# Kernel tuning notes

Hardware: AMD Instinct MI355X
Metric: run time of the kernel (lower is better)

The kernel has to match this reference:

```python
import jax, jax.numpy as jnp
import numpy as np

B, S, IN, H = 32, 512, 512, 1024

def setup_inputs() -> dict:
    key = jax.random.key(0)
    ks = jax.random.split(key, 13)
    sx = 1.0 / np.sqrt(IN)
    sh = 1.0 / np.sqrt(H)
    inp = {"x": jax.random.normal(ks[0], (B, S, IN), dtype=jnp.float32)}
    names_x = ["wxf", "wxi", "wxo", "wxc"]
    names_h = ["whf", "whi", "who", "whc"]
    names_b = ["bhf", "bhi", "bho", "bhc"]
    for j in range(4):
        inp[names_x[j]] = jax.random.uniform(ks[1 + j], (IN, H), dtype=jnp.float32, minval=-sx, maxval=sx)
        inp[names_h[j]] = jax.random.uniform(ks[5 + j], (H, H), dtype=jnp.float32, minval=-sh, maxval=sh)
        inp[names_b[j]] = jax.random.uniform(ks[9 + j], (H,), dtype=jnp.float32, minval=-sh, maxval=sh)
    return inp

def reference(x, wxf, whf, bhf, wxi, whi, bhi, wxo, who, bho, wxc, whc, bhc):
    b = x.shape[0]
    h = whf.shape[0]
    # Precompute all input projections (no bias on w_x_*): [S, B, 4H]
    wx = jnp.concatenate([wxf, wxi, wxo, wxc], axis=1)          # [IN, 4H]
    gx = jnp.einsum("bsi,ig->sbg", x, wx)                        # [S, B, 4H]
    wh = jnp.concatenate([whf, whi, who, whc], axis=1)           # [H, 4H]
    bh = jnp.concatenate([bhf, bhi, bho, bhc], axis=0)           # [4H]

    h0 = jnp.zeros((b, h), dtype=x.dtype)
    c0 = jnp.zeros((b, h), dtype=x.dtype)

    def step(carry, gxt):
        ht, ct = carry
        gates = gxt + ht @ wh + bh                               # [B, 4H]
        ft, it, ot, ch = jnp.split(jax.nn.sigmoid(gates), 4, axis=-1)
        # NOTE: original uses sigmoid (not tanh) for the candidate cell ct_hat
        ct_new = ft * ct + it * ch
        ht_new = ot * jnp.tanh(ct_new)
        # NOTE: original appends the output gate ot (not ht) to the sequence
        return (ht_new, ct_new), ot

    (ht, ct), outs = jax.lax.scan(step, (h0, c0), gx)
    return jnp.transpose(outs, (1, 0, 2)), (ht, ct)
```

## Files before the change

### kernel.cpp

```cpp
#include <hip/hip_runtime.h>
#include <stdint.h>


typedef short bf16x8 __attribute__((ext_vector_type(8)));
typedef float f32x4  __attribute__((ext_vector_type(4)));
typedef unsigned int uint4v __attribute__((ext_vector_type(4)));

#define MFMA16(a, b, c) __builtin_amdgcn_mfma_f32_16x16x32_bf16((a), (b), (c), 0, 0, 0)

__device__ __forceinline__ unsigned short f2bf(float f) {
    unsigned int u = __builtin_bit_cast(unsigned int, f);
    u = (u + 0x7FFFu + ((u >> 16) & 1u)) >> 16;
    return (unsigned short)u;
}
__device__ __forceinline__ float bf2f(unsigned short h) {
    unsigned int u = ((unsigned int)h) << 16;
    return __builtin_bit_cast(float, u);
}
__device__ __forceinline__ float sigmoidf_(float x) { return 1.0f / (1.0f + __expf(-x)); }
__device__ __forceinline__ float tanhf_(float x)    { return 1.0f - 2.0f / (__expf(2.0f * x) + 1.0f); }

__global__ void __launch_bounds__(256) gx_gemm(
    const float* __restrict__ X,
    const float* __restrict__ Wf, const float* __restrict__ Wi,
    const float* __restrict__ Wo, const float* __restrict__ Wc,
    unsigned short* __restrict__ gxOut)
{
    __shared__ unsigned short As[128 * 40];
    __shared__ unsigned short Bs[128 * 40];

    const int tid  = threadIdx.x;
    const int lane = tid & 63;
    const int wid  = tid >> 6;
    const int lr   = lane & 15;
    const int lq   = lane >> 4;

    const int m0 = blockIdx.x * 128;
    const int n0 = blockIdx.y * 128;
    const float* Wg = (n0 < 1024) ? Wf : (n0 < 2048) ? Wi : (n0 < 3072) ? Wo : Wc;
    const int ncol0 = n0 & 1023;

    const int mw = (wid & 1) * 64;
    const int nw = (wid >> 1) * 64;

    f32x4 acc[4][4];
#pragma unroll
    for (int i = 0; i < 4; i++)
#pragma unroll
        for (int j = 0; j < 4; j++) acc[i][j] = (f32x4){0.f, 0.f, 0.f, 0.f};

    for (int k0 = 0; k0 < 512; k0 += 32) {
#pragma unroll
        for (int i = 0; i < 4; i++) {
            int s   = tid + i * 256;
            int row = s >> 3;
            int c4  = s & 7;
            float4 v = *(const float4*)(X + (size_t)(m0 + row) * 512 + k0 + c4 * 4);
            ushort4 h;
            h.x = f2bf(v.x); h.y = f2bf(v.y); h.z = f2bf(v.z); h.w = f2bf(v.w);
            *(ushort4*)(As + row * 40 + c4 * 4) = h;
        }
#pragma unroll
        for (int i = 0; i < 4; i++) {
            int s  = tid + i * 256;
            int kk = s >> 5;
            int c4 = s & 31;
            float4 v = *(const float4*)(Wg + (size_t)(k0 + kk) * 1024 + ncol0 + c4 * 4);
            Bs[(c4 * 4 + 0) * 40 + kk] = f2bf(v.x);
            Bs[(c4 * 4 + 1) * 40 + kk] = f2bf(v.y);
            Bs[(c4 * 4 + 2) * 40 + kk] = f2bf(v.z);
            Bs[(c4 * 4 + 3) * 40 + kk] = f2bf(v.w);
        }
        __syncthreads();

        bf16x8 af[4], bfr[4];
#pragma unroll
        for (int tm = 0; tm < 4; tm++)
            af[tm] = *(const bf16x8*)(As + (mw + tm * 16 + lr) * 40 + lq * 8);
#pragma unroll
        for (int tn = 0; tn < 4; tn++)
            bfr[tn] = *(const bf16x8*)(Bs + (nw + tn * 16 + lr) * 40 + lq * 8);
#pragma unroll
        for (int tm = 0; tm < 4; tm++)
#pragma unroll
            for (int tn = 0; tn < 4; tn++)
                acc[tm][tn] = MFMA16(af[tm], bfr[tn], acc[tm][tn]);
        __syncthreads();
    }

#pragma unroll
    for (int tm = 0; tm < 4; tm++)
#pragma unroll
        for (int tn = 0; tn < 4; tn++)
#pragma unroll
            for (int r = 0; r < 4; r++) {
                int row = m0 + mw + tm * 16 + lq * 4 + r;
                int col = n0 + nw + tn * 16 + lr;
                gxOut[(size_t)row * 4096 + col] = f2bf(acc[tm][tn][r]);
            }
}

#define NWG 128
#define LDS2_BYTES 41216
#define GBUF 5120
#define KSTR 1280
#define CSTR 20

__global__ void __launch_bounds__(256, 1) lstm_scan(
    const float* __restrict__ Whf, const float* __restrict__ Whi,
    const float* __restrict__ Who, const float* __restrict__ Whc,
    const float* __restrict__ Bf,  const float* __restrict__ Bi,
    const float* __restrict__ Bo,  const float* __restrict__ Bc,
    const unsigned short* __restrict__ gx,
    unsigned short* __restrict__ hhist,
    float* __restrict__ out)
{
    extern __shared__ char lds[];
    float* glds = (float*)lds;
    float* blds = (float*)(lds + 40960);

    const int tid  = threadIdx.x;
    const int w    = blockIdx.x;
    const int bg   = w >> 6;
    const int cg   = w & 63;
    const int j0   = cg * 16;
    const int lane = tid & 63;
    const int kq   = tid >> 6;
    const int lr   = lane & 15;
    const int lq   = lane >> 4;

    if (tid < 64) {
        int g = tid >> 4, jj = tid & 15;
        const float* bp = (g == 0) ? Bf : (g == 1) ? Bi : (g == 2) ? Bo : Bc;
        blds[tid] = bp[j0 + jj];
    }

    bf16x8 bfrag[4][8];
#pragma unroll
    for (int g = 0; g < 4; g++) {
        const float* wp = (g == 0) ? Whf : (g == 1) ? Whi : (g == 2) ? Who : Whc;
#pragma unroll
        for (int ks = 0; ks < 8; ks++) {
            int kbase = kq * 256 + ks * 32 + lq * 8;
            bf16x8 b;
#pragma unroll
            for (int j = 0; j < 8; j++)
                b[j] = (short)f2bf(wp[(size_t)(kbase + j) * 1024 + j0 + lr]);
            bfrag[g][ks] = b;
        }
    }

    const int cb = tid >> 4;
    const int cj = tid & 15;
    const int b  = bg * 16 + cb;
    float c_reg = 0.f;

    __syncthreads();

    for (int t = 0; t < 512; t++) {
        float* gb = glds + (t & 1) * GBUF;

        const unsigned short* gxr = gx + ((size_t)(b * 512 + t)) * 4096 + j0 + cj;
        float gxv[4];
#pragma unroll
        for (int g = 0; g < 4; g++) gxv[g] = bf2f(gxr[(size_t)g * 1024]);

        if (t > 0) {
            const unsigned short* hsrc = hhist + (size_t)t * 32768;

            f32x4 acc[4];
#pragma unroll
            for (int g = 0; g < 4; g++) acc[g] = (f32x4){0.f, 0.f, 0.f, 0.f};

            uint4v fa[8];
            unsigned int pend = 0xFFu;
            while (pend) {
#pragma unroll
                for (int ks = 0; ks < 8; ks++) {
                    if (pend & (1u << ks)) {
                        const unsigned short* p = hsrc + (bg * 16 + lr) * 1024
                                                   + kq * 256 + ks * 32 + lq * 8;
                        asm volatile("global_load_dwordx4 %0, %1, off sc0 sc1"
                                     : "=v"(fa[ks]) : "v"(p));
                    }
                }
                asm volatile("s_waitcnt vmcnt(0)" ::: "memory");
                __builtin_amdgcn_sched_barrier(0);

                unsigned int np = 0;
#pragma unroll
                for (int ks = 0; ks < 8; ks++) {
                    if (pend & (1u << ks)) {
                        uint4v u = fa[ks];
                        bool dirty = (u[0] == 0xFFFFFFFFu) | (u[1] == 0xFFFFFFFFu)
                                   | (u[2] == 0xFFFFFFFFu) | (u[3] == 0xFFFFFFFFu);
                        if (__any(dirty)) {
                            np |= 1u << ks;
                        } else {
                            bf16x8 a = __builtin_bit_cast(bf16x8, u);
                            acc[0] = MFMA16(a, bfrag[0][ks], acc[0]);
                            acc[1] = MFMA16(a, bfrag[1][ks], acc[1]);
                            acc[2] = MFMA16(a, bfrag[2][ks], acc[2]);
                            acc[3] = MFMA16(a, bfrag[3][ks], acc[3]);
                        }
                    }
                }
                pend = np;
            }

#pragma unroll
            for (int g = 0; g < 4; g++)
                *(f32x4*)(gb + kq * KSTR + (g * 16 + lr) * CSTR + lq * 4) = acc[g];
        }
        __syncthreads();

        float sg[4];
#pragma unroll
        for (int g = 0; g < 4; g++) {
            float dot = 0.f;
            if (t > 0) {
#pragma unroll
                for (int p = 0; p < 4; p++)
                    dot += gb[p * KSTR + (g * 16 + cj) * CSTR + cb];
            }
            sg[g] = sigmoidf_(dot + gxv[g] + blds[g * 16 + cj]);
        }
        float cn = sg[0] * c_reg + sg[1] * sg[3];
        c_reg = cn;
        float hn = sg[2] * tanhf_(cn);

        if (t < 511) {
            unsigned int hb = (unsigned int)f2bf(hn);
            unsigned int nb = (unsigned int)__shfl_xor((int)hb, 1);
            unsigned int v  = (hb & 0xFFFFu) | (nb << 16);
            unsigned int v2 = (unsigned int)__shfl_xor((int)v, 2);
            unsigned int v4 = (unsigned int)__shfl_xor((int)v, 4);
            unsigned int v6 = (unsigned int)__shfl_xor((int)v2, 4);
            if ((cj & 7) == 0) {
                uint4v q;
                q[0] = v; q[1] = v2; q[2] = v4; q[3] = v6;
                unsigned short* dst = hhist + (size_t)(t + 1) * 32768
                                      + b * 1024 + j0 + cj;
                asm volatile("global_store_dwordx4 %0, %1, off sc1"
                             :: "v"(dst), "v"(q) : "memory");
            }
            out[((size_t)b * 512 + t) * 1024 + j0 + cj] = sg[2];
        } else {
            out[((size_t)b * 512 + t) * 1024 + j0 + cj] = sg[2];
            out[16777216 + b * 1024 + j0 + cj]          = hn;
            out[16777216 + 32768 + b * 1024 + j0 + cj]  = cn;
        }
    }
}

__global__ void ws_diag(float* out, float mb) { out[threadIdx.x] = -mb; }

extern "C" void kernel_launch(void* const* d_in, const int* in_sizes, int n_in,
                              void* d_out, int out_size, void* d_ws, size_t ws_size,
                              hipStream_t stream)
{
    const float* x   = (const float*)d_in[0];
    const float* wxf = (const float*)d_in[1];
    const float* whf = (const float*)d_in[2];
    const float* bhf = (const float*)d_in[3];
    const float* wxi = (const float*)d_in[4];
    const float* whi = (const float*)d_in[5];
    const float* bhi = (const float*)d_in[6];
    const float* wxo = (const float*)d_in[7];
    const float* who = (const float*)d_in[8];
    const float* bho = (const float*)d_in[9];
    const float* wxc = (const float*)d_in[10];
    const float* whc = (const float*)d_in[11];
    const float* bhc = (const float*)d_in[12];
    float* out = (float*)d_out;

    const size_t GX_BYTES = (size_t)16384 * 4096 * 2;
    const size_t HH_BYTES = (size_t)512 * 32 * 1024 * 2;
    const size_t NEED = GX_BYTES + HH_BYTES;

    if (ws_size < NEED) {
        ws_diag<<<dim3(1), dim3(256), 0, stream>>>(out, (float)(ws_size >> 20));
        return;
    }

    unsigned short* gxbuf = (unsigned short*)d_ws;
    unsigned short* hh    = (unsigned short*)((char*)d_ws + GX_BYTES);

    (void)hipFuncSetAttribute((const void*)lstm_scan,
                              hipFuncAttributeMaxDynamicSharedMemorySize, LDS2_BYTES);

    gx_gemm<<<dim3(128, 32), dim3(256), 0, stream>>>(x, wxf, wxi, wxo, wxc, gxbuf);
    hipMemsetAsync(hh, 0xFF, HH_BYTES, stream);
    lstm_scan<<<dim3(NWG), dim3(256), LDS2_BYTES, stream>>>(
        whf, whi, who, whc, bhf, bhi, bho, bhc, gxbuf, hh, out);
}
```

Before: 2.627 ms.

## Halve scan workgroups to 64 with 512 threads and 32 hidden columns each

Measured after the change: 2.440 ms. 7.1% less time.

```diff
diff --git a/kernel.cpp b/kernel.cpp
--- a/kernel.cpp
+++ b/kernel.cpp
@@ -100,13 +100,12 @@
             }
 }
 
-#define NWG 128
-#define LDS2_BYTES 41216
-#define GBUF 5120
-#define KSTR 1280
+#define NWG 64
+#define LDS2_BYTES 82432
+#define KSTR 2560
 #define CSTR 20
 
-__global__ void __launch_bounds__(256, 1) lstm_scan(
+__global__ void __launch_bounds__(512, 1) lstm_scan(
     const float* __restrict__ Whf, const float* __restrict__ Whi,
     const float* __restrict__ Who, const float* __restrict__ Whc,
     const float* __restrict__ Bf,  const float* __restrict__ Bi,
@@ -117,49 +116,49 @@
 {
     extern __shared__ char lds[];
     float* glds = (float*)lds;
-    float* blds = (float*)(lds + 40960);
+    float* blds = (float*)(lds + 81920);
 
     const int tid  = threadIdx.x;
     const int w    = blockIdx.x;
-    const int bg   = w >> 6;
-    const int cg   = w & 63;
-    const int j0   = cg * 16;
+    const int bg   = w & 1;
+    const int cg   = w >> 1;
+    const int j0   = cg * 32;
     const int lane = tid & 63;
     const int kq   = tid >> 6;
     const int lr   = lane & 15;
     const int lq   = lane >> 4;
 
-    if (tid < 64) {
-        int g = tid >> 4, jj = tid & 15;
+    if (tid < 128) {
+        int g = tid >> 5, jj = tid & 31;
         const float* bp = (g == 0) ? Bf : (g == 1) ? Bi : (g == 2) ? Bo : Bc;
         blds[tid] = bp[j0 + jj];
     }
 
-    bf16x8 bfrag[4][8];
-#pragma unroll
-    for (int g = 0; g < 4; g++) {
+    bf16x8 bfrag[8][4];
+#pragma unroll
+    for (int ct = 0; ct < 8; ct++) {
+        int c = ct * 16 + lr;
+        int g = c >> 5, jj = c & 31;
         const float* wp = (g == 0) ? Whf : (g == 1) ? Whi : (g == 2) ? Who : Whc;
 #pragma unroll
-        for (int ks = 0; ks < 8; ks++) {
-            int kbase = kq * 256 + ks * 32 + lq * 8;
+        for (int ks = 0; ks < 4; ks++) {
+            int kbase = kq * 128 + ks * 32 + lq * 8;
             bf16x8 b;
 #pragma unroll
             for (int j = 0; j < 8; j++)
-                b[j] = (short)f2bf(wp[(size_t)(kbase + j) * 1024 + j0 + lr]);
-            bfrag[g][ks] = b;
-        }
-    }
-
-    const int cb = tid >> 4;
-    const int cj = tid & 15;
+                b[j] = (short)f2bf(wp[(size_t)(kbase + j) * 1024 + j0 + jj]);
+            bfrag[ct][ks] = b;
+        }
+    }
+
+    const int cb = tid >> 5;
+    const int cj = tid & 31;
     const int b  = bg * 16 + cb;
     float c_reg = 0.f;
 
     __syncthreads();
 
     for (int t = 0; t < 512; t++) {
-        float* gb = glds + (t & 1) * GBUF;
-
         const unsigned short* gxr = gx + ((size_t)(b * 512 + t)) * 4096 + j0 + cj;
         float gxv[4];
 #pragma unroll
@@ -168,18 +167,18 @@
         if (t > 0) {
             const unsigned short* hsrc = hhist + (size_t)t * 32768;
 
-            f32x4 acc[4];
-#pragma unroll
-            for (int g = 0; g < 4; g++) acc[g] = (f32x4){0.f, 0.f, 0.f, 0.f};
-
-            uint4v fa[8];
-            unsigned int pend = 0xFFu;
+            f32x4 acc[8];
+#pragma unroll
+            for (int ct = 0; ct < 8; ct++) acc[ct] = (f32x4){0.f, 0.f, 0.f, 0.f};
+
+            uint4v fa[4];
+            unsigned int pend = 0xFu;
             while (pend) {
 #pragma unroll
-                for (int ks = 0; ks < 8; ks++) {
+                for (int ks = 0; ks < 4; ks++) {
                     if (pend & (1u << ks)) {
                         const unsigned short* p = hsrc + (bg * 16 + lr) * 1024
-                                                   + kq * 256 + ks * 32 + lq * 8;
+                                                   + kq * 128 + ks * 32 + lq * 8;
                         asm volatile("global_load_dwordx4 %0, %1, off sc0 sc1"
                                      : "=v"(fa[ks]) : "v"(p));
                     }
@@ -189,7 +188,7 @@
 
                 unsigned int np = 0;
 #pragma unroll
-                for (int ks = 0; ks < 8; ks++) {
+                for (int ks = 0; ks < 4; ks++) {
                     if (pend & (1u << ks)) {
                         uint4v u = fa[ks];
                         bool dirty = (u[0] == 0xFFFFFFFFu) | (u[1] == 0xFFFFFFFFu)
@@ -198,10 +197,9 @@
                             np |= 1u << ks;
                         } else {
                             bf16x8 a = __builtin_bit_cast(bf16x8, u);
-                            acc[0] = MFMA16(a, bfrag[0][ks], acc[0]);
-                            acc[1] = MFMA16(a, bfrag[1][ks], acc[1]);
-                            acc[2] = MFMA16(a, bfrag[2][ks], acc[2]);
-                            acc[3] = MFMA16(a, bfrag[3][ks], acc[3]);
+#pragma unroll
+                            for (int ct = 0; ct < 8; ct++)
+                                acc[ct] = MFMA16(a, bfrag[ct][ks], acc[ct]);
                         }
                     }
                 }
@@ -209,8 +207,9 @@
             }
 
 #pragma unroll
-            for (int g = 0; g < 4; g++)
-                *(f32x4*)(gb + kq * KSTR + (g * 16 + lr) * CSTR + lq * 4) = acc[g];
+            for (int ct = 0; ct < 8; ct++)
+                *(f32x4*)(glds + kq * KSTR + (ct * 16 + lr) * CSTR + lq * 4)
+                    = acc[ct];
         }
         __syncthreads();
 
@@ -220,10 +219,10 @@
             float dot = 0.f;
             if (t > 0) {
 #pragma unroll
-                for (int p = 0; p < 4; p++)
-                    dot += gb[p * KSTR + (g * 16 + cj) * CSTR + cb];
-            }
-            sg[g] = sigmoidf_(dot + gxv[g] + blds[g * 16 + cj]);
+                for (int p = 0; p < 8; p++)
+                    dot += glds[p * KSTR + (g * 32 + cj) * CSTR + cb];
+            }
+            sg[g] = sigmoidf_(dot + gxv[g] + blds[g * 32 + cj]);
         }
         float cn = sg[0] * c_reg + sg[1] * sg[3];
         c_reg = cn;
@@ -250,6 +249,7 @@
             out[16777216 + b * 1024 + j0 + cj]          = hn;
             out[16777216 + 32768 + b * 1024 + j0 + cj]  = cn;
         }
+        __syncthreads();
     }
 }
 
@@ -291,6 +291,6 @@
 
     gx_gemm<<<dim3(128, 32), dim3(256), 0, stream>>>(x, wxf, wxi, wxo, wxc, gxbuf);
     hipMemsetAsync(hh, 0xFF, HH_BYTES, stream);
-    lstm_scan<<<dim3(NWG), dim3(256), LDS2_BYTES, stream>>>(
+    lstm_scan<<<dim3(NWG), dim3(512), LDS2_BYTES, stream>>>(
         whf, whi, who, whc, bhf, bhi, bho, bhc, gxbuf, hh, out);
 }
```
